# Kernel tuning notes

Measured on AMD Instinct MI355X. Metric: run time of the kernel, lower is better.

Reference implementation:

```python
import jax, jax.numpy as jnp
import numpy as np

L = 512
Z_DIM = 128
C = 128
EPS = 1e-5


def _ln(x, g, b):
    m = jnp.mean(x, axis=-1, keepdims=True)
    v = jnp.var(x, axis=-1, keepdims=True)
    return (x - m) * jax.lax.rsqrt(v + EPS) * g + b


def setup_inputs() -> dict:
    key = jax.random.key(0)
    ks = jax.random.split(key, 12)
    s_z = 1.0 / np.sqrt(Z_DIM)
    s_c = 1.0 / np.sqrt(C)
    return {
        "z": jax.random.normal(ks[0], (L, L, Z_DIM), dtype=jnp.float32),
        "norm_g": jnp.ones((Z_DIM,), jnp.float32),
        "norm_b": jnp.zeros((Z_DIM,), jnp.float32),
        "a_w": jax.random.normal(ks[1], (C, Z_DIM), jnp.float32) * s_z,
        "a_b": jnp.zeros((C,), jnp.float32),
        "ag_w": jax.random.normal(ks[2], (C, Z_DIM), jnp.float32) * s_z,
        "ag_b": jnp.zeros((C,), jnp.float32),
        "onorm_g": jnp.ones((C,), jnp.float32),
        "onorm_b": jnp.zeros((C,), jnp.float32),
        "o_w": jax.random.normal(ks[3], (Z_DIM, C), jnp.float32) * s_c,
        "o_b": jnp.zeros((Z_DIM,), jnp.float32),
        "g_w": jax.random.normal(ks[4], (Z_DIM, Z_DIM), jnp.float32) * s_z,
        "g_b": jnp.zeros((Z_DIM,), jnp.float32),
    }


def reference(z, norm_g, norm_b, a_w, a_b, ag_w, ag_b, onorm_g, onorm_b, o_w, o_b, g_w, g_b):
    zn = _ln(z, norm_g, norm_b)                                   # [L, L, z_dim]
    # gated projection; source computes b identically to a (alinear/aglinear for both)
    a = (zn @ a_w.T + a_b) * jax.nn.sigmoid(zn @ ag_w.T + ag_b)   # [L, L, c]
    o = jnp.einsum('ilc,jlc->ijc', a, a)                          # [L, L, c]
    o = _ln(o, onorm_g, onorm_b)
    o = o @ o_w.T + o_b                                           # [L, L, z_dim]
    return o * jax.nn.sigmoid(zn @ g_w.T + g_b)
```

## Files before the change

kernel.cpp:

```cpp
#include <hip/hip_runtime.h>
#include <stdint.h>

typedef unsigned short bf16;
typedef __attribute__((ext_vector_type(8))) short short8;
typedef __attribute__((ext_vector_type(4))) float f32x4;

#define MFMA16(a, b, c) __builtin_amdgcn_mfma_f32_16x16x32_bf16((a), (b), (c), 0, 0, 0)

__device__ __forceinline__ bf16 f2bf(float f) {
    unsigned u = __float_as_uint(f);
    u += 0x7fffu + ((u >> 16) & 1u);
    return (bf16)(u >> 16);
}
__device__ __forceinline__ float bf2f(bf16 s) { return __uint_as_float(((unsigned)s) << 16); }

__device__ __forceinline__ void gload_lds16(const void* g, void* lds) {
    auto gp = (const __attribute__((address_space(1))) unsigned int*)(uintptr_t)g;
    auto lp = (__attribute__((address_space(3))) unsigned int*)(uintptr_t)lds;
    __builtin_amdgcn_global_load_lds(gp, lp, 16, 0, 0);
}

__global__ __launch_bounds__(256) void k_wconv(const float* __restrict__ aw,
                                               const float* __restrict__ agw,
                                               const float* __restrict__ gw,
                                               const float* __restrict__ ow,
                                               bf16* __restrict__ wbf,
                                               bf16* __restrict__ owbf) {
    int i = blockIdx.x * 256 + threadIdx.x;
    int m = i >> 14, k = i & 16383;
    const float* s = (m == 0) ? aw : (m == 1) ? agw : (m == 2) ? gw : ow;
    float v = s[k];
    if (m < 3) wbf[i] = f2bf(v); else owbf[k] = f2bf(v);
}

__global__ __launch_bounds__(256) void k_ln_proj(const float* __restrict__ z,
                                                 const float* __restrict__ ng,
                                                 const float* __restrict__ nb,
                                                 const float* __restrict__ ab,
                                                 const float* __restrict__ agb,
                                                 const float* __restrict__ gbv,
                                                 const bf16* __restrict__ wbf,
                                                 bf16* __restrict__ a_t,
                                                 bf16* __restrict__ gbuf) {
    __shared__ bf16 zn_s[64 * 136];
    __shared__ bf16 w_s[128 * 136];
    __shared__ float ng_s[128], nb_s[128];

    const int t = threadIdx.x;
    const int r0 = blockIdx.x * 64;
    bf16* st = w_s;

    if (t < 128) { ng_s[t] = ng[t]; nb_s[t] = nb[t]; }

    {
        int row = t >> 2, q = t & 3;
        const float* zp = z + (size_t)(r0 + row) * 128 + q * 32;
        float x[32];
        float s = 0.f, ss = 0.f;
#pragma unroll
        for (int i = 0; i < 8; ++i) {
            float4 v = ((const float4*)zp)[i];
            x[4 * i + 0] = v.x; x[4 * i + 1] = v.y; x[4 * i + 2] = v.z; x[4 * i + 3] = v.w;
        }
#pragma unroll
        for (int i = 0; i < 32; ++i) { s += x[i]; ss += x[i] * x[i]; }
        s += __shfl_xor(s, 1); ss += __shfl_xor(ss, 1);
        s += __shfl_xor(s, 2); ss += __shfl_xor(ss, 2);
        float mean = s * (1.f / 128.f);
        float var = ss * (1.f / 128.f) - mean * mean;
        float rstd = rsqrtf(var + 1e-5f);
        __syncthreads();
#pragma unroll
        for (int i = 0; i < 32; ++i) {
            int c = q * 32 + i;
            zn_s[row * 136 + c] = f2bf((x[i] - mean) * rstd * ng_s[c] + nb_s[c]);
        }
    }

    const int lane = t & 63, w = t >> 6;
    const int lr = lane & 15, quad = lane >> 4;
    const int arow = w * 16 + lr;

    auto stage_w = [&](int mat) {
        const uint4* src = (const uint4*)(wbf + mat * 16384);
#pragma unroll
        for (int i = 0; i < 8; ++i) {
            int idx = t + i * 256;
            int row = idx >> 4, part = idx & 15;
            *(uint4*)&w_s[row * 136 + part * 8] = src[idx];
        }
    };
    auto gemmv = [&](f32x4* acc) {
#pragma unroll
        for (int kk = 0; kk < 4; ++kk) {
            short8 af = *(const short8*)&zn_s[arow * 136 + kk * 32 + quad * 8];
#pragma unroll
            for (int nt = 0; nt < 8; ++nt) {
                short8 bfr = *(const short8*)&w_s[(nt * 16 + lr) * 136 + kk * 32 + quad * 8];
                acc[nt] = MFMA16(af, bfr, acc[nt]);
            }
        }
    };

    f32x4 zero4 = {0.f, 0.f, 0.f, 0.f};
    f32x4 acc_a[8], acc_b[8];
#pragma unroll
    for (int nt = 0; nt < 8; ++nt) { acc_a[nt] = zero4; acc_b[nt] = zero4; }

    stage_w(0);
    __syncthreads();
    gemmv(acc_a);
    __syncthreads();
    stage_w(1);
    __syncthreads();
    gemmv(acc_b);
    __syncthreads();

#pragma unroll
    for (int nt = 0; nt < 8; ++nt) {
        int c = nt * 16 + lr;
        float abv = ab[c], agbv = agb[c];
#pragma unroll
        for (int r = 0; r < 4; ++r) {
            int row = w * 16 + quad * 4 + r;
            float av = acc_a[nt][r] + abv;
            float agvv = acc_b[nt][r] + agbv;
            st[c * 64 + row] = f2bf(av * (1.f / (1.f + __expf(-agvv))));
        }
    }
    __syncthreads();
#pragma unroll
    for (int i = 0; i < 4; ++i) {
        int idx = t + i * 256;
        int c = idx >> 3, part = idx & 7;
        *(uint4*)(a_t + (size_t)c * 262144 + r0 + part * 8) = *(const uint4*)&st[c * 64 + part * 8];
    }
    __syncthreads();

    stage_w(2);
    __syncthreads();
#pragma unroll
    for (int nt = 0; nt < 8; ++nt) acc_a[nt] = zero4;
    gemmv(acc_a);
    __syncthreads();
#pragma unroll
    for (int nt = 0; nt < 8; ++nt) {
        int c = nt * 16 + lr;
        float gb0 = gbv[c];
#pragma unroll
        for (int r = 0; r < 4; ++r) {
            int row = w * 16 + quad * 4 + r;
            float v = acc_a[nt][r] + gb0;
            st[row * 128 + c] = f2bf(1.f / (1.f + __expf(-v)));
        }
    }
    __syncthreads();
#pragma unroll
    for (int i = 0; i < 4; ++i) {
        int idx = t + i * 256;
        int row = idx >> 4, part = idx & 15;
        *(uint4*)(gbuf + (size_t)(r0 + row) * 128 + part * 8) = *(const uint4*)&st[row * 128 + part * 8];
    }
}

__global__ __launch_bounds__(256) void k_einsum(const bf16* __restrict__ a_t,
                                                bf16* __restrict__ o_t) {
    __shared__ bf16 smem[16384];
    bf16* As = smem;
    bf16* Bs = smem + 8192;

    const int t = threadIdx.x;
    const int bx = blockIdx.x;
    const int c = bx >> 4;
    const int ti = (bx >> 2) & 3, tj = bx & 3;
    const int i0 = ti * 128, j0 = tj * 128;
    const size_t cbase = (size_t)c * 262144;
    const bf16* Ac = a_t + cbase;

    const int lane = t & 63, w = t >> 6;
    const int lr = lane & 15, quad = lane >> 4;
    const int wi = w >> 1, wj = w & 1;

    f32x4 zero4 = {0.f, 0.f, 0.f, 0.f};
    f32x4 acc[4][4];
#pragma unroll
    for (int mt = 0; mt < 4; ++mt)
#pragma unroll
        for (int nt = 0; nt < 4; ++nt) acc[mt][nt] = zero4;

    for (int kb = 0; kb < 8; ++kb) {
        __syncthreads();
#pragma unroll
        for (int q = 0; q < 4; ++q) {
            int t16 = (w << 8) + (q << 6) + lane;
            int row = t16 >> 3;
            int cb = t16 & 7;
            int cbg = cb ^ (row & 7);
            int gcol = kb * 64 + cbg * 8;
            gload_lds16(Ac + (size_t)(i0 + row) * 512 + gcol, As + (((w << 8) + (q << 6)) << 3));
            gload_lds16(Ac + (size_t)(j0 + row) * 512 + gcol, Bs + (((w << 8) + (q << 6)) << 3));
        }
        __syncthreads();
#pragma unroll
        for (int kk8 = 0; kk8 < 8; kk8 += 4) {
            short8 af[4], bfr[4];
#pragma unroll
            for (int mt = 0; mt < 4; ++mt) {
                int r = wi * 64 + mt * 16 + lr;
                af[mt] = *(const short8*)&As[r * 64 + (((kk8 + quad) ^ (lr & 7)) << 3)];
            }
#pragma unroll
            for (int nt = 0; nt < 4; ++nt) {
                int r = wj * 64 + nt * 16 + lr;
                bfr[nt] = *(const short8*)&Bs[r * 64 + (((kk8 + quad) ^ (lr & 7)) << 3)];
            }
#pragma unroll
            for (int mt = 0; mt < 4; ++mt)
#pragma unroll
                for (int nt = 0; nt < 4; ++nt)
                    acc[mt][nt] = MFMA16(af[mt], bfr[nt], acc[mt][nt]);
        }
    }

    __syncthreads();
    bf16* Cs = smem;
#pragma unroll
    for (int mt = 0; mt < 4; ++mt)
#pragma unroll
        for (int nt = 0; nt < 4; ++nt)
#pragma unroll
            for (int r = 0; r < 4; ++r) {
                int il = wi * 64 + mt * 16 + quad * 4 + r;
                int jl = wj * 64 + nt * 16 + lr;
                Cs[il * 128 + jl] = f2bf(acc[mt][nt][r]);
            }
    __syncthreads();
    bf16* Oc = o_t + cbase;
#pragma unroll
    for (int i = 0; i < 8; ++i) {
        int idx = t + (i << 8);
        int row = idx >> 4, part = idx & 15;
        *(uint4*)(Oc + (size_t)(i0 + row) * 512 + j0 + part * 8) = *(const uint4*)&Cs[row * 128 + part * 8];
    }
}

__global__ __launch_bounds__(256) void k_out(const bf16* __restrict__ o_t,
                                             const bf16* __restrict__ gbuf,
                                             const float* __restrict__ og,
                                             const float* __restrict__ ob,
                                             const bf16* __restrict__ owbf,
                                             const float* __restrict__ obias,
                                             float* __restrict__ out) {
    __shared__ bf16 pool[128 * 136];
    __shared__ float og_s[128], ob_s[128], obi_s[128];
    bf16* ot_s = pool;
    bf16* n_s = pool;

    const int t = threadIdx.x;
    const int p0 = blockIdx.x * 128;
    if (t < 128) { og_s[t] = og[t]; ob_s[t] = ob[t]; obi_s[t] = obias[t]; }

#pragma unroll
    for (int i = 0; i < 8; ++i) {
        int idx = t + (i << 8);
        int c = idx >> 4, part = idx & 15;
        *(uint4*)&ot_s[c * 128 + part * 8] = *(const uint4*)(o_t + (size_t)c * 262144 + p0 + part * 8);
    }
    __syncthreads();

    {
        int col = t >> 1, h = t & 1;
        float s = 0.f, ss = 0.f;
        float xv[64];
#pragma unroll
        for (int k = 0; k < 64; ++k) {
            float x = bf2f(ot_s[(h * 64 + k) * 128 + col]);
            xv[k] = x; s += x; ss += x * x;
        }
        s += __shfl_xor(s, 1); ss += __shfl_xor(ss, 1);
        float mean = s * (1.f / 128.f);
        float var = ss * (1.f / 128.f) - mean * mean;
        float rstd = rsqrtf(var + 1e-5f);
        __syncthreads();
#pragma unroll
        for (int k = 0; k < 64; ++k) {
            int cc = h * 64 + k;
            n_s[col * 136 + cc] = f2bf((xv[k] - mean) * rstd * og_s[cc] + ob_s[cc]);
        }
    }
    __syncthreads();

    const int lane = t & 63, w = t >> 6;
    const int lr = lane & 15, quad = lane >> 4;
    f32x4 zero4 = {0.f, 0.f, 0.f, 0.f};
    f32x4 acc[2][8];
#pragma unroll
    for (int mt = 0; mt < 2; ++mt)
#pragma unroll
        for (int nt = 0; nt < 8; ++nt) acc[mt][nt] = zero4;

#pragma unroll
    for (int kk = 0; kk < 4; ++kk) {
        short8 af[2];
#pragma unroll
        for (int mt = 0; mt < 2; ++mt)
            af[mt] = *(const short8*)&n_s[(w * 32 + mt * 16 + lr) * 136 + kk * 32 + quad * 8];
#pragma unroll
        for (int nt = 0; nt < 8; ++nt) {
            short8 bfr = *(const short8*)(owbf + (nt * 16 + lr) * 128 + kk * 32 + quad * 8);
            acc[0][nt] = MFMA16(af[0], bfr, acc[0][nt]);
            acc[1][nt] = MFMA16(af[1], bfr, acc[1][nt]);
        }
    }

#pragma unroll
    for (int mt = 0; mt < 2; ++mt)
#pragma unroll
        for (int nt = 0; nt < 8; ++nt) {
            int zd = nt * 16 + lr;
            float bias = obi_s[zd];
#pragma unroll
            for (int r = 0; r < 4; ++r) {
                int m = w * 32 + mt * 16 + quad * 4 + r;
                size_t off = (size_t)(p0 + m) * 128 + zd;
                out[off] = (acc[mt][nt][r] + bias) * bf2f(gbuf[off]);
            }
        }
}

extern "C" void kernel_launch(void* const* d_in, const int* in_sizes, int n_in,
                              void* d_out, int out_size, void* d_ws, size_t ws_size,
                              hipStream_t stream) {
    (void)in_sizes; (void)n_in; (void)out_size; (void)ws_size;
    const float* z   = (const float*)d_in[0];
    const float* ng  = (const float*)d_in[1];
    const float* nb  = (const float*)d_in[2];
    const float* aw  = (const float*)d_in[3];
    const float* ab  = (const float*)d_in[4];
    const float* agw = (const float*)d_in[5];
    const float* agb = (const float*)d_in[6];
    const float* ong = (const float*)d_in[7];
    const float* onb = (const float*)d_in[8];
    const float* ow  = (const float*)d_in[9];
    const float* obi = (const float*)d_in[10];
    const float* gw  = (const float*)d_in[11];
    const float* gbb = (const float*)d_in[12];

    char* ws = (char*)d_ws;
    bf16* wbf  = (bf16*)(ws);
    bf16* owbf = (bf16*)(ws + 98304);
    bf16* a_t  = (bf16*)(ws + 131072);
    bf16* gbuf = (bf16*)(ws + 131072 + 67108864);
    bf16* o_t  = (bf16*)(ws + 131072 + 2 * 67108864);

    k_wconv<<<256, 256, 0, stream>>>(aw, agw, gw, ow, wbf, owbf);
    k_ln_proj<<<4096, 256, 0, stream>>>(z, ng, nb, ab, agb, gbb, wbf, a_t, gbuf);
    k_einsum<<<2048, 256, 0, stream>>>(a_t, o_t);
    k_out<<<2048, 256, 0, stream>>>(o_t, gbuf, ong, onb, owbf, obi, (float*)d_out);
}
```

Measured before the change: 423.1 us.

## Exploit einsum symmetry, double-buffer einsum loads, swizzle LN-proj LDS staging

The einsum output is symmetric in i and j, so only the upper-triangular 128x128 tiles are computed (10 of 16 per channel). Each off-diagonal tile is written twice, once transposed, and diagonal tiles load a single operand. The einsum K loop now double-buffers global-to-LDS loads so the next slice is fetched while the current one is multiplied. Separately, the LN/projection kernel keeps normalized rows in registers, loads weights with direct-to-LDS async copies into XOR-swizzled unpadded layouts, and packs bf16 stores. The costs are extra transpose writes, more LDS per block, and branchy tile indexing.

```diff
diff --git a/kernel.cpp b/kernel.cpp
--- a/kernel.cpp
+++ b/kernel.cpp
@@ -13,6 +13,10 @@
     return (bf16)(u >> 16);
 }
 __device__ __forceinline__ float bf2f(bf16 s) { return __uint_as_float(((unsigned)s) << 16); }
+__device__ __forceinline__ unsigned pack2(float a, float b) {
+    return ((unsigned)f2bf(a)) | (((unsigned)f2bf(b)) << 16);
+}
+__device__ __forceinline__ float sigmoidf_(float x) { return 1.f / (1.f + __expf(-x)); }
 
 __device__ __forceinline__ void gload_lds16(const void* g, void* lds) {
     auto gp = (const __attribute__((address_space(1))) unsigned int*)(uintptr_t)g;
@@ -42,20 +46,18 @@
                                                  const bf16* __restrict__ wbf,
                                                  bf16* __restrict__ a_t,
                                                  bf16* __restrict__ gbuf) {
-    __shared__ bf16 zn_s[64 * 136];
-    __shared__ bf16 w_s[128 * 136];
-    __shared__ float ng_s[128], nb_s[128];
+    __shared__ bf16 zn_s[64 * 128];
+    __shared__ bf16 w_s[128 * 128];
 
     const int t = threadIdx.x;
     const int r0 = blockIdx.x * 64;
-    bf16* st = w_s;
-
-    if (t < 128) { ng_s[t] = ng[t]; nb_s[t] = nb[t]; }
-
+    const int lane = t & 63, w = t >> 6;
+    const int lr = lane & 15, quad = lane >> 4;
+    const int row = w * 16 + lr;
+
+    float x[32];
     {
-        int row = t >> 2, q = t & 3;
-        const float* zp = z + (size_t)(r0 + row) * 128 + q * 32;
-        float x[32];
+        const float* zp = z + (size_t)(r0 + row) * 128 + quad * 32;
         float s = 0.f, ss = 0.f;
 #pragma unroll
         for (int i = 0; i < 8; ++i) {
@@ -64,40 +66,66 @@
         }
 #pragma unroll
         for (int i = 0; i < 32; ++i) { s += x[i]; ss += x[i] * x[i]; }
-        s += __shfl_xor(s, 1); ss += __shfl_xor(ss, 1);
-        s += __shfl_xor(s, 2); ss += __shfl_xor(ss, 2);
+        s += __shfl_xor(s, 16); ss += __shfl_xor(ss, 16);
+        s += __shfl_xor(s, 32); ss += __shfl_xor(ss, 32);
         float mean = s * (1.f / 128.f);
         float var = ss * (1.f / 128.f) - mean * mean;
         float rstd = rsqrtf(var + 1e-5f);
-        __syncthreads();
-#pragma unroll
-        for (int i = 0; i < 32; ++i) {
-            int c = q * 32 + i;
-            zn_s[row * 136 + c] = f2bf((x[i] - mean) * rstd * ng_s[c] + nb_s[c]);
-        }
-    }
-
-    const int lane = t & 63, w = t >> 6;
-    const int lr = lane & 15, quad = lane >> 4;
-    const int arow = w * 16 + lr;
+#pragma unroll
+        for (int i = 0; i < 8; ++i) {
+            float4 g4 = ((const float4*)(ng + quad * 32))[i];
+            float4 b4 = ((const float4*)(nb + quad * 32))[i];
+            x[4 * i + 0] = (x[4 * i + 0] - mean) * rstd * g4.x + b4.x;
+            x[4 * i + 1] = (x[4 * i + 1] - mean) * rstd * g4.y + b4.y;
+            x[4 * i + 2] = (x[4 * i + 2] - mean) * rstd * g4.z + b4.z;
+            x[4 * i + 3] = (x[4 * i + 3] - mean) * rstd * g4.w + b4.w;
+        }
+    }
+    {
+        unsigned zd[16];
+#pragma unroll
+        for (int j = 0; j < 16; ++j) zd[j] = pack2(x[2 * j], x[2 * j + 1]);
+#pragma unroll
+        for (int i = 0; i < 4; ++i) {
+            int c = quad * 4 + i;
+            int pos = (c & 8) | ((c & 7) ^ (row & 7));
+            uint4 d; d.x = zd[4 * i]; d.y = zd[4 * i + 1]; d.z = zd[4 * i + 2]; d.w = zd[4 * i + 3];
+            *(uint4*)&zn_s[row * 128 + pos * 8] = d;
+        }
+    }
 
     auto stage_w = [&](int mat) {
-        const uint4* src = (const uint4*)(wbf + mat * 16384);
+        const bf16* src = wbf + mat * 16384;
 #pragma unroll
         for (int i = 0; i < 8; ++i) {
-            int idx = t + i * 256;
-            int row = idx >> 4, part = idx & 15;
-            *(uint4*)&w_s[row * 136 + part * 8] = src[idx];
+            int idx = i * 256 + t;
+            int rw = idx >> 4, c = idx & 15;
+            int csrc = (c & 8) | ((c & 7) ^ (rw & 7));
+            gload_lds16(src + rw * 128 + csrc * 8, w_s + idx * 8);
         }
     };
-    auto gemmv = [&](f32x4* acc) {
+
+    stage_w(0);
+    __syncthreads();
+
+    short8 af[4];
+#pragma unroll
+    for (int kk = 0; kk < 4; ++kk) {
+        int c = kk * 4 + quad;
+        int pos = (c & 8) | ((c & 7) ^ (row & 7));
+        af[kk] = *(const short8*)&zn_s[row * 128 + pos * 8];
+    }
+
+    auto gemm = [&](f32x4* acc) {
 #pragma unroll
         for (int kk = 0; kk < 4; ++kk) {
-            short8 af = *(const short8*)&zn_s[arow * 136 + kk * 32 + quad * 8];
+            int c = kk * 4 + quad;
 #pragma unroll
             for (int nt = 0; nt < 8; ++nt) {
-                short8 bfr = *(const short8*)&w_s[(nt * 16 + lr) * 136 + kk * 32 + quad * 8];
-                acc[nt] = MFMA16(af, bfr, acc[nt]);
+                int rw = nt * 16 + lr;
+                int pos = (c & 8) | ((c & 7) ^ (rw & 7));
+                short8 bfr = *(const short8*)&w_s[rw * 128 + pos * 8];
+                acc[nt] = MFMA16(af[kk], bfr, acc[nt]);
             }
         }
     };
@@ -107,72 +135,68 @@
 #pragma unroll
     for (int nt = 0; nt < 8; ++nt) { acc_a[nt] = zero4; acc_b[nt] = zero4; }
 
-    stage_w(0);
-    __syncthreads();
-    gemmv(acc_a);
+    gemm(acc_a);
     __syncthreads();
     stage_w(1);
     __syncthreads();
-    gemmv(acc_b);
-    __syncthreads();
-
+    gemm(acc_b);
+    __syncthreads();
+
+    bf16* st_a = w_s;
 #pragma unroll
     for (int nt = 0; nt < 8; ++nt) {
         int c = nt * 16 + lr;
         float abv = ab[c], agbv = agb[c];
-#pragma unroll
-        for (int r = 0; r < 4; ++r) {
-            int row = w * 16 + quad * 4 + r;
-            float av = acc_a[nt][r] + abv;
-            float agvv = acc_b[nt][r] + agbv;
-            st[c * 64 + row] = f2bf(av * (1.f / (1.f + __expf(-agvv))));
-        }
+        float v0 = (acc_a[nt][0] + abv) * sigmoidf_(acc_b[nt][0] + agbv);
+        float v1 = (acc_a[nt][1] + abv) * sigmoidf_(acc_b[nt][1] + agbv);
+        float v2 = (acc_a[nt][2] + abv) * sigmoidf_(acc_b[nt][2] + agbv);
+        float v3 = (acc_a[nt][3] + abv) * sigmoidf_(acc_b[nt][3] + agbv);
+        uint2 d; d.x = pack2(v0, v1); d.y = pack2(v2, v3);
+        *(uint2*)&st_a[c * 72 + w * 16 + quad * 4] = d;
     }
     __syncthreads();
 #pragma unroll
     for (int i = 0; i < 4; ++i) {
-        int idx = t + i * 256;
+        int idx = i * 256 + t;
         int c = idx >> 3, part = idx & 7;
-        *(uint4*)(a_t + (size_t)c * 262144 + r0 + part * 8) = *(const uint4*)&st[c * 64 + part * 8];
-    }
-    __syncthreads();
-
+        *(uint4*)(a_t + (size_t)c * 262144 + r0 + part * 8) = *(const uint4*)&st_a[c * 72 + part * 8];
+    }
+    __syncthreads();
     stage_w(2);
     __syncthreads();
 #pragma unroll
     for (int nt = 0; nt < 8; ++nt) acc_a[nt] = zero4;
-    gemmv(acc_a);
-    __syncthreads();
+    gemm(acc_a);
+
+    bf16* st_g = zn_s;
 #pragma unroll
     for (int nt = 0; nt < 8; ++nt) {
         int c = nt * 16 + lr;
         float gb0 = gbv[c];
 #pragma unroll
-        for (int r = 0; r < 4; ++r) {
-            int row = w * 16 + quad * 4 + r;
-            float v = acc_a[nt][r] + gb0;
-            st[row * 128 + c] = f2bf(1.f / (1.f + __expf(-v)));
-        }
+        for (int r = 0; r < 4; ++r)
+            st_g[(w * 16 + quad * 4 + r) * 128 + c] = f2bf(sigmoidf_(acc_a[nt][r] + gb0));
     }
     __syncthreads();
 #pragma unroll
     for (int i = 0; i < 4; ++i) {
-        int idx = t + i * 256;
-        int row = idx >> 4, part = idx & 15;
-        *(uint4*)(gbuf + (size_t)(r0 + row) * 128 + part * 8) = *(const uint4*)&st[row * 128 + part * 8];
+        int idx = i * 256 + t;
+        int rr = idx >> 4, part = idx & 15;
+        *(uint4*)(gbuf + (size_t)(r0 + rr) * 128 + part * 8) = *(const uint4*)&st_g[rr * 128 + part * 8];
     }
 }
 
 __global__ __launch_bounds__(256) void k_einsum(const bf16* __restrict__ a_t,
                                                 bf16* __restrict__ o_t) {
-    __shared__ bf16 smem[16384];
-    bf16* As = smem;
-    bf16* Bs = smem + 8192;
+    __shared__ bf16 smem[32768];
 
     const int t = threadIdx.x;
     const int bx = blockIdx.x;
-    const int c = bx >> 4;
-    const int ti = (bx >> 2) & 3, tj = bx & 3;
+    const int c = bx / 10;
+    const int pi = bx - c * 10;
+    const int ti = (pi < 4) ? 0 : (pi < 7) ? 1 : (pi < 9) ? 2 : 3;
+    const int tj = pi - ((pi < 4) ? 0 : (pi < 7) ? 3 : (pi < 9) ? 5 : 6);
+    const bool diag = (ti == tj);
     const int i0 = ti * 128, j0 = tj * 128;
     const size_t cbase = (size_t)c * 262144;
     const bf16* Ac = a_t + cbase;
@@ -181,6 +205,19 @@
     const int lr = lane & 15, quad = lane >> 4;
     const int wi = w >> 1, wj = w & 1;
 
+    auto stage = [&](int kb, int buf) {
+        bf16* As = smem + buf * 16384;
+        bf16* Bs = As + 8192;
+#pragma unroll
+        for (int q = 0; q < 4; ++q) {
+            int t16 = (w << 8) + (q << 6) + lane;
+            int rw = t16 >> 3, cb = t16 & 7;
+            int gcol = (kb << 6) + ((cb ^ (rw & 7)) << 3);
+            gload_lds16(Ac + (size_t)(i0 + rw) * 512 + gcol, As + t16 * 8);
+            if (!diag) gload_lds16(Ac + (size_t)(j0 + rw) * 512 + gcol, Bs + t16 * 8);
+        }
+    };
+
     f32x4 zero4 = {0.f, 0.f, 0.f, 0.f};
     f32x4 acc[4][4];
 #pragma unroll
@@ -188,32 +225,21 @@
 #pragma unroll
         for (int nt = 0; nt < 4; ++nt) acc[mt][nt] = zero4;
 
+    stage(0, 0);
     for (int kb = 0; kb < 8; ++kb) {
         __syncthreads();
-#pragma unroll
-        for (int q = 0; q < 4; ++q) {
-            int t16 = (w << 8) + (q << 6) + lane;
-            int row = t16 >> 3;
-            int cb = t16 & 7;
-            int cbg = cb ^ (row & 7);
-            int gcol = kb * 64 + cbg * 8;
-            gload_lds16(Ac + (size_t)(i0 + row) * 512 + gcol, As + (((w << 8) + (q << 6)) << 3));
-            gload_lds16(Ac + (size_t)(j0 + row) * 512 + gcol, Bs + (((w << 8) + (q << 6)) << 3));
-        }
-        __syncthreads();
+        if (kb < 7) stage(kb + 1, (kb + 1) & 1);
+        const bf16* As = smem + (kb & 1) * 16384;
+        const bf16* Bs = diag ? As : As + 8192;
 #pragma unroll
         for (int kk8 = 0; kk8 < 8; kk8 += 4) {
             short8 af[4], bfr[4];
 #pragma unroll
-            for (int mt = 0; mt < 4; ++mt) {
-                int r = wi * 64 + mt * 16 + lr;
-                af[mt] = *(const short8*)&As[r * 64 + (((kk8 + quad) ^ (lr & 7)) << 3)];
-            }
-#pragma unroll
-            for (int nt = 0; nt < 4; ++nt) {
-                int r = wj * 64 + nt * 16 + lr;
-                bfr[nt] = *(const short8*)&Bs[r * 64 + (((kk8 + quad) ^ (lr & 7)) << 3)];
-            }
+            for (int mt = 0; mt < 4; ++mt)
+                af[mt] = *(const short8*)&As[(wi * 64 + mt * 16 + lr) * 64 + (((kk8 + quad) ^ (lr & 7)) << 3)];
+#pragma unroll
+            for (int nt = 0; nt < 4; ++nt)
+                bfr[nt] = *(const short8*)&Bs[(wj * 64 + nt * 16 + lr) * 64 + (((kk8 + quad) ^ (lr & 7)) << 3)];
 #pragma unroll
             for (int mt = 0; mt < 4; ++mt)
 #pragma unroll
@@ -224,6 +250,7 @@
 
     __syncthreads();
     bf16* Cs = smem;
+    bf16* Oc = o_t + cbase;
 #pragma unroll
     for (int mt = 0; mt < 4; ++mt)
 #pragma unroll
@@ -232,15 +259,34 @@
             for (int r = 0; r < 4; ++r) {
                 int il = wi * 64 + mt * 16 + quad * 4 + r;
                 int jl = wj * 64 + nt * 16 + lr;
-                Cs[il * 128 + jl] = f2bf(acc[mt][nt][r]);
+                Cs[il * 136 + jl] = f2bf(acc[mt][nt][r]);
             }
     __syncthreads();
-    bf16* Oc = o_t + cbase;
 #pragma unroll
     for (int i = 0; i < 8; ++i) {
-        int idx = t + (i << 8);
-        int row = idx >> 4, part = idx & 15;
-        *(uint4*)(Oc + (size_t)(i0 + row) * 512 + j0 + part * 8) = *(const uint4*)&Cs[row * 128 + part * 8];
+        int idx = (i << 8) + t;
+        int rw = idx >> 4, part = idx & 15;
+        *(uint4*)(Oc + (size_t)(i0 + rw) * 512 + j0 + part * 8) = *(const uint4*)&Cs[rw * 136 + part * 8];
+    }
+    if (!diag) {
+        __syncthreads();
+#pragma unroll
+        for (int mt = 0; mt < 4; ++mt)
+#pragma unroll
+            for (int nt = 0; nt < 4; ++nt)
+#pragma unroll
+                for (int r = 0; r < 4; ++r) {
+                    int il = wi * 64 + mt * 16 + quad * 4 + r;
+                    int jl = wj * 64 + nt * 16 + lr;
+                    Cs[jl * 136 + il] = f2bf(acc[mt][nt][r]);
+                }
+        __syncthreads();
+#pragma unroll
+        for (int i = 0; i < 8; ++i) {
+            int idx = (i << 8) + t;
+            int rw = idx >> 4, part = idx & 15;
+            *(uint4*)(Oc + (size_t)(j0 + rw) * 512 + i0 + part * 8) = *(const uint4*)&Cs[rw * 136 + part * 8];
+        }
     }
 }
 
@@ -253,8 +299,6 @@
                                              float* __restrict__ out) {
     __shared__ bf16 pool[128 * 136];
     __shared__ float og_s[128], ob_s[128], obi_s[128];
-    bf16* ot_s = pool;
-    bf16* n_s = pool;
 
     const int t = threadIdx.x;
     const int p0 = blockIdx.x * 128;
@@ -262,19 +306,19 @@
 
 #pragma unroll
     for (int i = 0; i < 8; ++i) {
-        int idx = t + (i << 8);
+        int idx = (i << 8) + t;
         int c = idx >> 4, part = idx & 15;
-        *(uint4*)&ot_s[c * 128 + part * 8] = *(const uint4*)(o_t + (size_t)c * 262144 + p0 + part * 8);
+        *(uint4*)&pool[c * 136 + part * 8] = *(const uint4*)(o_t + (size_t)c * 262144 + p0 + part * 8);
     }
     __syncthreads();
 
     {
         int col = t >> 1, h = t & 1;
+        float xv[64];
         float s = 0.f, ss = 0.f;
-        float xv[64];
 #pragma unroll
         for (int k = 0; k < 64; ++k) {
-            float x = bf2f(ot_s[(h * 64 + k) * 128 + col]);
+            float x = bf2f(pool[(h * 64 + k) * 136 + col]);
             xv[k] = x; s += x; ss += x * x;
         }
         s += __shfl_xor(s, 1); ss += __shfl_xor(ss, 1);
@@ -285,7 +329,7 @@
 #pragma unroll
         for (int k = 0; k < 64; ++k) {
             int cc = h * 64 + k;
-            n_s[col * 136 + cc] = f2bf((xv[k] - mean) * rstd * og_s[cc] + ob_s[cc]);
+            pool[col * 136 + cc] = f2bf((xv[k] - mean) * rstd * og_s[cc] + ob_s[cc]);
         }
     }
     __syncthreads();
@@ -304,7 +348,7 @@
         short8 af[2];
 #pragma unroll
         for (int mt = 0; mt < 2; ++mt)
-            af[mt] = *(const short8*)&n_s[(w * 32 + mt * 16 + lr) * 136 + kk * 32 + quad * 8];
+            af[mt] = *(const short8*)&pool[(w * 32 + mt * 16 + lr) * 136 + kk * 32 + quad * 8];
 #pragma unroll
         for (int nt = 0; nt < 8; ++nt) {
             short8 bfr = *(const short8*)(owbf + (nt * 16 + lr) * 128 + kk * 32 + quad * 8);
@@ -355,6 +399,6 @@
 
     k_wconv<<<256, 256, 0, stream>>>(aw, agw, gw, ow, wbf, owbf);
     k_ln_proj<<<4096, 256, 0, stream>>>(z, ng, nb, ab, agb, gbb, wbf, a_t, gbuf);
-    k_einsum<<<2048, 256, 0, stream>>>(a_t, o_t);
+    k_einsum<<<1280, 256, 0, stream>>>(a_t, o_t);
     k_out<<<2048, 256, 0, stream>>>(o_t, gbuf, ong, onb, owbf, obi, (float*)d_out);
 }
```

Result: no change. 428.4 us (+1.2%).
